# Kernel tuning notes

Hardware: AMD Instinct MI355X
Metric: run time of the kernel (lower is better)

The kernel has to match this reference:

```python
import jax, jax.numpy as jnp
import numpy as np
import math

D_MODEL = 1024
NHEAD = 16
D_FF = 4096
MAX_LEN = 512
LN_EPS = 1e-5


def setup_inputs() -> dict:
    key = jax.random.key(0)
    ks = jax.random.split(key, 12)
    d, h, dff, L = D_MODEL, NHEAD, D_FF, MAX_LEN
    B, S = 16, 512
    s = lambda k, shape, std: jax.random.normal(k, shape, dtype=jnp.float32) * std
    return {
        "x": s(ks[0], (B, S, d), 1.0),
        "in_proj_w": s(ks[1], (3 * d, d), d ** -0.5),   # torch MHA in_proj_weight
        "in_proj_b": jnp.zeros((3 * d,), jnp.float32),
        "out_w": s(ks[2], (d, d), d ** -0.5),            # out_proj.weight (out,in)
        "out_b": jnp.zeros((d,), jnp.float32),
        "rel_bias": s(ks[3], (h, 2 * L - 1), 0.02),      # (nhead, 2*max_len-1)
        "w1": s(ks[4], (dff, d), d ** -0.5),             # Linear(d, dff).weight
        "b1": jnp.zeros((dff,), jnp.float32),
        "w2": s(ks[5], (d, dff), dff ** -0.5),           # Linear(dff, d).weight
        "b2": jnp.zeros((d,), jnp.float32),
        "ln1_w": jnp.ones((d,), jnp.float32),
        "ln1_b": jnp.zeros((d,), jnp.float32),
        "ln2_w": jnp.ones((d,), jnp.float32),
        "ln2_b": jnp.zeros((d,), jnp.float32),
    }


def _layernorm(x, w, b):
    mu = jnp.mean(x, axis=-1, keepdims=True)
    var = jnp.mean(jnp.square(x - mu), axis=-1, keepdims=True)
    return (x - mu) * jax.lax.rsqrt(var + LN_EPS) * w + b


def _rel_pos_bias(rel_bias, seq_len):
    pos = jnp.arange(seq_len)
    rel = pos[:, None] - pos[None, :] + (MAX_LEN - 1)        # (S,S)
    rel = jnp.clip(rel, 0, 2 * MAX_LEN - 2)
    return rel_bias[:, rel]                                  # (H,S,S)


def reference(x, in_proj_w, in_proj_b, out_w, out_b, rel_bias,
              w1, b1, w2, b2, ln1_w, ln1_b, ln2_w, ln2_b):
    B, S, d = x.shape
    h = NHEAD
    hd = d // h
    bias = _rel_pos_bias(rel_bias, S)[None]                  # (1,H,S,S)

    # --- attention block (pre-norm) ---
    residual = x
    xn = _layernorm(x, ln1_w, ln1_b)
    qkv = xn @ in_proj_w.T + in_proj_b                       # (B,S,3d)
    q, k, v = jnp.split(qkv, 3, axis=-1)
    q = q.reshape(B, S, h, hd).transpose(0, 2, 1, 3)         # (B,H,S,hd)
    k = k.reshape(B, S, h, hd).transpose(0, 2, 1, 3)
    v = v.reshape(B, S, h, hd).transpose(0, 2, 1, 3)
    scores = jnp.einsum('bhqd,bhkd->bhqk', q, k) / math.sqrt(hd) + bias
    probs = jax.nn.softmax(scores, axis=-1)
    attn = jnp.einsum('bhqk,bhkd->bhqd', probs, v)           # (B,H,S,hd)
    attn = attn.transpose(0, 2, 1, 3).reshape(B, S, d)
    attn = attn @ out_w.T + out_b
    x = residual + attn

    # --- FFN block (pre-norm) ---
    residual = x
    xn = _layernorm(x, ln2_w, ln2_b)
    hdn = jax.nn.gelu(xn @ w1.T + b1, approximate=False)
    x = residual + hdn @ w2.T + b2
    return x
```

## Files before the change

kernel.cpp:

```cpp
#include <hip/hip_runtime.h>
#include <hip/hip_bf16.h>
#include <stdint.h>

typedef __hip_bfloat16 bf16;
typedef __attribute__((ext_vector_type(8))) __bf16 bf16x8;
typedef __attribute__((ext_vector_type(4))) float f32x4;

#define D_MODEL 1024
#define NHEAD   16
#define HDIM    64
#define DFF     4096
#define BATCH   16
#define SEQ     512
#define MROWS   (BATCH*SEQ)

__device__ __forceinline__ float b2f_bits(unsigned short u) {
    return __uint_as_float(((unsigned)u) << 16);
}
__device__ __forceinline__ bf16 f2b(float v) { return __float2bfloat16(v); }
__device__ __forceinline__ unsigned short f2b_bits(float v) {
    bf16 t = __float2bfloat16(v);
    return *(unsigned short*)&t;
}
__device__ __forceinline__ void gll16(void* lds, const void* gsrc) {
    __builtin_amdgcn_global_load_lds(
        (const __attribute__((address_space(1))) unsigned*)gsrc,
        (__attribute__((address_space(3))) unsigned*)lds,
        16, 0, 0);
}
__device__ __forceinline__ float gelu_f(float u) {
    float z  = 0.7978845608028654f * (u + 0.044715f * u * u * u);
    float az = fabsf(z);
    float e  = __expf(-2.0f * az);
    float th = (1.0f - e) / (1.0f + e);
    th = copysignf(th, z);
    return 0.5f * u * (1.0f + th);
}

__global__ __launch_bounds__(256)
void cvt_kernel(const float* __restrict__ in, bf16* __restrict__ out, int n)
{
    int i = (blockIdx.x * 256 + threadIdx.x) * 4;
    if (i >= n) return;
    float4 f = *(const float4*)(in + i);
    ushort4 o;
    o.x = f2b_bits(f.x); o.y = f2b_bits(f.y);
    o.z = f2b_bits(f.z); o.w = f2b_bits(f.w);
    *(ushort4*)((unsigned short*)out + i) = o;
}

__global__ __launch_bounds__(256)
void ln_kernel(const float* __restrict__ xin, const float* __restrict__ w,
               const float* __restrict__ b, bf16* __restrict__ out)
{
    int row  = blockIdx.x;
    int t    = threadIdx.x;
    int lane = t & 63, wv = t >> 6;
    int col  = t * 4;

    float4 f = *(const float4*)(xin + (size_t)row * D_MODEL + col);
    float v[4] = {f.x, f.y, f.z, f.w};

    float s  = v[0] + v[1] + v[2] + v[3];
    float ss = v[0]*v[0] + v[1]*v[1] + v[2]*v[2] + v[3]*v[3];
    #pragma unroll
    for (int m = 1; m < 64; m <<= 1) {
        s  += __shfl_xor(s,  m, 64);
        ss += __shfl_xor(ss, m, 64);
    }
    __shared__ float rs0[4], rs1[4];
    if (lane == 0) { rs0[wv] = s; rs1[wv] = ss; }
    __syncthreads();
    s  = rs0[0] + rs0[1] + rs0[2] + rs0[3];
    ss = rs1[0] + rs1[1] + rs1[2] + rs1[3];

    float mu  = s * (1.0f / D_MODEL);
    float var = ss * (1.0f / D_MODEL) - mu * mu;
    float rs  = rsqrtf(var + 1e-5f);

    float4 wf = *(const float4*)(w + col);
    float4 bf = *(const float4*)(b + col);
    ushort4 o;
    o.x = f2b_bits((v[0]-mu)*rs*wf.x + bf.x);
    o.y = f2b_bits((v[1]-mu)*rs*wf.y + bf.y);
    o.z = f2b_bits((v[2]-mu)*rs*wf.z + bf.z);
    o.w = f2b_bits((v[3]-mu)*rs*wf.w + bf.w);
    *(ushort4*)((unsigned short*)out + (size_t)row * D_MODEL + col) = o;
}

template<int EPI, bool OUT_B16>
__global__ __launch_bounds__(256)
void gemm_bt(const bf16* __restrict__ A, const bf16* __restrict__ Bw,
             const float* __restrict__ bias, const float* __restrict__ resid,
             void* __restrict__ Cout, bf16* __restrict__ qb,
             bf16* __restrict__ ktb, bf16* __restrict__ vb,
             int M, int N, int K)
{
    int t    = threadIdx.x;
    int lane = t & 63, w = t >> 6;
    int wm   = w & 1,  wn = w >> 1;
    int q    = lane >> 4, r = lane & 15;

    int gx  = gridDim.x;
    int L   = blockIdx.y * gx + blockIdx.x;
    int qq  = (gx * gridDim.y) >> 3;
    int nid = (L & 7) * qq + (L >> 3);
    int mb  = (nid / gx) * 128, nb = (nid % gx) * 128;

    __shared__ char smem[32768];

    f32x4 acc[4][4] = {};

    const char* Ag = (const char*)((const unsigned short*)A + (size_t)mb * K);
    const char* Bg = (const char*)((const unsigned short*)Bw + (size_t)nb * K);

    int ar0 = t >> 2,  ac0 = (t & 3) << 3;

    int nt = K >> 5;

    #define STAGE(c, k0) do {                                      \
        char* dA = smem + (c) * 16384;                             \
        char* dB = dA + 8192;                                      \
        size_t off0 = ((size_t)ar0 * K + (k0) + ac0) * 2;          \
        size_t off1 = off0 + (size_t)64 * K * 2;                   \
        gll16(dA + t * 16,        Ag + off0);                      \
        gll16(dA + 4096 + t * 16, Ag + off1);                      \
        gll16(dB + t * 16,        Bg + off0);                      \
        gll16(dB + 4096 + t * 16, Bg + off1);                      \
    } while (0)

    STAGE(0, 0);
    __syncthreads();

    int cur = 0;
    for (int tt = 0; tt < nt; ++tt) {
        if (tt + 1 < nt) STAGE(cur ^ 1, (tt + 1) << 5);

        const __bf16* Asb = (const __bf16*)(smem + cur * 16384);
        const __bf16* Bsb = Asb + 4096;
        bf16x8 af[4], bfr[4];
        #pragma unroll
        for (int i = 0; i < 4; i++)
            af[i] = *(const bf16x8*)(Asb + (wm * 64 + i * 16 + r) * 32 + q * 8);
        #pragma unroll
        for (int j = 0; j < 4; j++)
            bfr[j] = *(const bf16x8*)(Bsb + (wn * 64 + j * 16 + r) * 32 + q * 8);
        #pragma unroll
        for (int i = 0; i < 4; i++)
            #pragma unroll
            for (int j = 0; j < 4; j++)
                acc[i][j] = __builtin_amdgcn_mfma_f32_16x16x32_bf16(af[i], bfr[j], acc[i][j], 0, 0, 0);

        __syncthreads();
        cur ^= 1;
    }
    #undef STAGE

    if (OUT_B16 && EPI != 3) {
        __bf16* Cs = (__bf16*)smem;
        #pragma unroll
        for (int j = 0; j < 4; j++) {
            int n = nb + wn * 64 + j * 16 + r;
            float bv = bias[n];
            #pragma unroll
            for (int i = 0; i < 4; i++) {
                #pragma unroll
                for (int rr = 0; rr < 4; rr++) {
                    float v = acc[i][j][rr] + bv;
                    if (EPI == 1) v = gelu_f(v);
                    if (EPI == 2) v += resid[(size_t)(mb + wm*64 + i*16 + q*4 + rr) * N + n];
                    unsigned short ub = f2b_bits(v);
                    Cs[(wm*64 + i*16 + q*4 + rr) * 128 + wn*64 + j*16 + r] = *(__bf16*)&ub;
                }
            }
        }
        __syncthreads();
        char* Cg = (char*)Cout;
        #pragma unroll
        for (int c = 0; c < 8; c++) {
            int idx = t + c * 256;
            int row = idx >> 4, ch = idx & 15;
            *(int4*)(Cg + ((size_t)(mb + row) * N + nb) * 2 + ch * 16) =
                *(const int4*)((const char*)Cs + row * 256 + ch * 16);
        }
    } else {
        #pragma unroll
        for (int j = 0; j < 4; j++) {
            int n = nb + wn * 64 + j * 16 + r;
            float bv = bias[n];
            #pragma unroll
            for (int i = 0; i < 4; i++) {
                int mbase = mb + wm * 64 + i * 16 + q * 4;
                #pragma unroll
                for (int rr = 0; rr < 4; rr++) {
                    int m = mbase + rr;
                    float v = acc[i][j][rr] + bv;
                    if (EPI == 1) v = gelu_f(v);
                    if (EPI == 2) v += resid[(size_t)m * N + n];
                    if (EPI == 3) {
                        int sect = n >> 10;
                        int h = (n >> 6) & 15;
                        int e = n & 63;
                        int bi = m >> 9, s = m & 511;
                        size_t bh = (size_t)bi * NHEAD + h;
                        bf16 val = f2b(v);
                        if (sect == 0)      qb[((bh * SEQ + s) << 6) + e] = val;
                        else if (sect == 1) ktb[((bh * SEQ + s) << 6) + e] = val;
                        else                vb[((bh * HDIM + e) << 9) + s] = val;
                    } else {
                        if (OUT_B16) ((bf16*)Cout)[(size_t)m * N + n] = f2b(v);
                        else         ((float*)Cout)[(size_t)m * N + n] = v;
                    }
                }
            }
        }
    }
}

__global__ __launch_bounds__(256, 3)
void attn_mfma(const bf16* __restrict__ Q, const bf16* __restrict__ K,
               const bf16* __restrict__ VT, const float* __restrict__ relb,
               bf16* __restrict__ out)
{
    int L   = blockIdx.x + (blockIdx.y << 3);
    int xcd = L & 7, jj = L >> 3;
    int bh  = xcd * 32 + (jj >> 3);
    int q0  = (jj & 7) * 64;
    int b   = bh >> 4, h = bh & 15;
    int t = threadIdx.x, lane = t & 63, w = t >> 6;
    int l15 = lane & 15, l4 = lane >> 4;

    __shared__ int4  kvbuf4[2048];
    __shared__ int4  Pls4[512];
    __shared__ float rbs[1024];

    char* kv = (char*)kvbuf4;
    char* Pb = (char*)Pls4;
    const char* Kg = (const char*)K  + ((size_t)bh << 16);
    const char* Vg = (const char*)VT + ((size_t)bh << 16);

    #define STAGE_KV(bs, c) do {                                              \
        char* kd = kv + (bs) * 16384;                                         \
        char* vd = kd + 8192;                                                 \
        _Pragma("unroll")                                                     \
        for (int i = 0; i < 2; i++) {                                         \
            int g = t + i * 256;                                              \
            int rr_ = g >> 3;                                                 \
            int jj_ = (g & 7) ^ (rr_ & 7);                                    \
            gll16(kd + g * 16,                                                \
                  Kg + (((size_t)(c) * 64 + rr_) << 7) + (jj_ << 4));         \
            gll16(vd + g * 16,                                                \
                  Vg + ((size_t)rr_ << 10) + ((size_t)(c) << 7) + (jj_ << 4));\
        }                                                                     \
    } while (0)

    const float* rb = relb + (size_t)h * (2 * SEQ - 1);
    for (int i = t; i < 2 * SEQ - 1; i += 256) rbs[i] = rb[i];
    STAGE_KV(0, 0);

    const unsigned short* Qp = (const unsigned short*)Q
        + (((size_t)bh * SEQ + q0 + w * 16 + l15) << 6) + l4 * 8;
    bf16x8 qf0 = *(const bf16x8*)Qp;
    bf16x8 qf1 = *(const bf16x8*)(Qp + 32);

    __syncthreads();

    int qbase  = q0 + w * 16 + l4 * 4;
    int prow   = w * 16 + l15;
    int prbase = prow << 7;
    int pswz   = (prow & 7) << 4;
    float sum[4] = {0.f, 0.f, 0.f, 0.f};
    f32x4 oacc[4] = {};

    int cur = 0;
    for (int c = 0; c < 8; ++c) {
        if (c < 7) STAGE_KV(cur ^ 1, c + 1);

        const char* Kl = kv + cur * 16384;
        const char* Vl = Kl + 8192;

        f32x4 sc[4];
        #pragma unroll
        for (int kt = 0; kt < 4; kt++) {
            int row = kt * 16 + l15;
            int swz = (row & 7) << 4;
            bf16x8 kf0 = *(const bf16x8*)(Kl + (((row << 7) + (l4 << 4)) ^ swz));
            bf16x8 kf1 = *(const bf16x8*)(Kl + (((row << 7) + 64 + (l4 << 4)) ^ swz));
            f32x4 a = {};
            a = __builtin_amdgcn_mfma_f32_16x16x32_bf16(qf0, kf0, a, 0, 0, 0);
            a = __builtin_amdgcn_mfma_f32_16x16x32_bf16(qf1, kf1, a, 0, 0, 0);
            sc[kt] = a;
        }

        #pragma unroll
        for (int kt = 0; kt < 4; kt++) {
            int relbase = qbase - (c * 64 + kt * 16 + l15) + (SEQ - 1);
            #pragma unroll
            for (int reg = 0; reg < 4; reg++) {
                float p = __expf(sc[kt][reg] * 0.125f + rbs[relbase + reg]);
                sum[reg] += p;
                float o = __shfl_xor(p, 1, 64);
                unsigned lo = f2b_bits((lane & 1) ? o : p);
                unsigned hi = f2b_bits((lane & 1) ? p : o);
                unsigned pk = lo | (hi << 16);
                if ((lane & 1) == (reg >> 1)) {
                    int row  = w * 16 + l4 * 4 + reg;
                    int byte = ((row << 7) + (kt << 5) + ((l15 & ~1) << 1))
                             ^ ((row & 7) << 4);
                    *(unsigned*)(Pb + byte) = pk;
                }
            }
        }

        #pragma unroll
        for (int k2 = 0; k2 < 2; k2++) {
            int pbyte = (prbase + (k2 << 6) + (l4 << 4)) ^ pswz;
            bf16x8 pf = *(const bf16x8*)(Pb + pbyte);
            #pragma unroll
            for (int et = 0; et < 4; et++) {
                int vrow = et * 16 + l15;
                bf16x8 vf = *(const bf16x8*)
                    (Vl + (((vrow << 7) + (k2 << 6) + (l4 << 4)) ^ ((vrow & 7) << 4)));
                oacc[et] = __builtin_amdgcn_mfma_f32_16x16x32_bf16(pf, vf, oacc[et], 0, 0, 0);
            }
        }

        __syncthreads();
        cur ^= 1;
    }
    #undef STAGE_KV

    #pragma unroll
    for (int m = 1; m < 16; m <<= 1)
        #pragma unroll
        for (int reg = 0; reg < 4; reg++)
            sum[reg] += __shfl_xor(sum[reg], m, 64);
    float rcp[4];
    #pragma unroll
    for (int reg = 0; reg < 4; reg++) rcp[reg] = 1.0f / sum[reg];

    bf16* op = out + (size_t)(b * SEQ + q0 + w * 16 + l4 * 4) * D_MODEL
             + h * HDIM + l15;
    #pragma unroll
    for (int et = 0; et < 4; et++)
        #pragma unroll
        for (int reg = 0; reg < 4; reg++)
            op[(size_t)reg * D_MODEL + et * 16] = f2b(oacc[et][reg] * rcp[reg]);
}

extern "C" void kernel_launch(void* const* d_in, const int* in_sizes, int n_in,
                              void* d_out, int out_size, void* d_ws, size_t ws_size,
                              hipStream_t stream)
{
    const float* x    = (const float*)d_in[0];
    const float* wqkv = (const float*)d_in[1];
    const float* bqkv = (const float*)d_in[2];
    const float* wo   = (const float*)d_in[3];
    const float* bo   = (const float*)d_in[4];
    const float* relb = (const float*)d_in[5];
    const float* w1   = (const float*)d_in[6];
    const float* b1   = (const float*)d_in[7];
    const float* w2   = (const float*)d_in[8];
    const float* b2   = (const float*)d_in[9];
    const float* ln1w = (const float*)d_in[10];
    const float* ln1b = (const float*)d_in[11];
    const float* ln2w = (const float*)d_in[12];
    const float* ln2b = (const float*)d_in[13];

    char* ws = (char*)d_ws;
    const size_t MB = 1048576;
    bf16*  wqkv_b = (bf16*)(ws + 1 * MB);
    bf16*  wo_b   = (bf16*)(ws + 7 * MB);
    bf16*  xn     = (bf16*)(ws + 9 * MB);
    bf16*  Qb     = (bf16*)(ws + 25 * MB);
    bf16*  Kb     = (bf16*)(ws + 41 * MB);
    float* x1     = (float*)(ws + 25 * MB);
    bf16*  w1_b   = (bf16*)(ws + 1 * MB);
    bf16*  w2_b   = (bf16*)(ws + 9 * MB);
    bf16*  xn2    = (bf16*)(ws + 9 * MB);
    bf16*  hid    = (bf16*)(ws + 57 * MB);
    bf16*  VT     = (bf16*)d_out;
    bf16*  att    = (bf16*)((char*)d_out + 16 * MB);
    float* out    = (float*)d_out;

    cvt_kernel<<<3072, 256, 0, stream>>>(wqkv, wqkv_b, 3 * D_MODEL * D_MODEL);
    cvt_kernel<<<1024, 256, 0, stream>>>(wo,   wo_b,   D_MODEL * D_MODEL);
    ln_kernel<<<MROWS, 256, 0, stream>>>(x, ln1w, ln1b, xn);
    gemm_bt<3,true><<<dim3(24, 64), 256, 0, stream>>>(xn, wqkv_b, bqkv, nullptr,
        nullptr, Qb, Kb, VT, MROWS, 3 * D_MODEL, D_MODEL);
    attn_mfma<<<dim3(8, 256), 256, 0, stream>>>(Qb, Kb, VT, relb, att);
    gemm_bt<2,false><<<dim3(8, 64), 256, 0, stream>>>(att, wo_b, bo, x,
        x1, nullptr, nullptr, nullptr, MROWS, D_MODEL, D_MODEL);
    cvt_kernel<<<4096, 256, 0, stream>>>(w1, w1_b, DFF * D_MODEL);
    ln_kernel<<<MROWS, 256, 0, stream>>>(x1, ln2w, ln2b, xn2);
    gemm_bt<1,true><<<dim3(32, 64), 256, 0, stream>>>(xn2, w1_b, b1, nullptr,
        hid, nullptr, nullptr, nullptr, MROWS, DFF, D_MODEL);
    cvt_kernel<<<4096, 256, 0, stream>>>(w2, w2_b, D_MODEL * DFF);
    gemm_bt<2,false><<<dim3(8, 64), 256, 0, stream>>>(hid, w2_b, b2, x1,
        out, nullptr, nullptr, nullptr, MROWS, D_MODEL, DFF);
}
```

Baseline: 518.4 us.

## Add 256x256-tile 8-wave GEMM with swizzled LDS for QKV and FFN1

Introduces a new GEMM kernel with 256x256 block tiles, 512 threads, double-buffered 128KB LDS, an XOR-swizzled LDS layout and interleaved half-tile prefetch with s_setprio around MFMA bursts. It replaces the 128x128 kernel for the QKV projection and the FFN first layer. The aim is more data reuse per LDS load, fewer bank conflicts and better overlap of loads with MFMA. In exchange, the large LDS footprint and high register use limit occupancy, and fewer blocks cover the grid.

Result: slower. 664.4 us (+28.2%).

```diff
diff --git a/kernel.cpp b/kernel.cpp
--- a/kernel.cpp
+++ b/kernel.cpp
@@ -88,13 +88,199 @@
     *(ushort4*)((unsigned short*)out + (size_t)row * D_MODEL + col) = o;
 }
 
+template<int EPI>
+__global__ __launch_bounds__(512, 2)
+void gemm8(const bf16* __restrict__ A, const bf16* __restrict__ Bw,
+           const float* __restrict__ bias, void* __restrict__ Cout,
+           bf16* __restrict__ qb, bf16* __restrict__ ktb,
+           bf16* __restrict__ vb, int M, int N, int K)
+{
+    constexpr int BUFSZ = 65536;
+    __shared__ char smem[131072];
+
+    int t = threadIdx.x;
+    int lane = t & 63, wid = t >> 6;
+    int wm = wid >> 2, wn = wid & 3;
+    int r = lane & 15, q = lane >> 4;
+
+    int gx  = gridDim.x;
+    int L   = blockIdx.y * gx + blockIdx.x;
+    int qq  = (gx * gridDim.y) >> 3;
+    int nid = (L & 7) * qq + (L >> 3);
+    int mb  = (nid / gx) * 256, nb = (nid % gx) * 256;
+
+    const char* Ag = (const char*)A + (size_t)mb * K * 2;
+    const char* Bg = (const char*)Bw + (size_t)nb * K * 2;
+
+    int g0r = t >> 2,   g0j = (t & 3) ^ ((g0r >> 1) & 3);
+    int g1r = g0r + 128, g1j = (t & 3) ^ ((g1r >> 1) & 3);
+    size_t a0 = (size_t)g0r * K * 2 + (size_t)g0j * 16;
+    size_t a1 = (size_t)g1r * K * 2 + (size_t)g1j * 16;
+
+    #define STG(mat, h, T, b) do {                                       \
+        char* d = smem + (b) * BUFSZ + (mat) * 32768 + (h) * 16384;      \
+        const char* s = (mat) ? Bg : Ag;                                 \
+        size_t ko = ((size_t)(T) * 64 + (h) * 32) * 2;                   \
+        gll16(d + t * 16,        s + a0 + ko);                           \
+        gll16(d + 8192 + t * 16, s + a1 + ko);                           \
+    } while (0)
+
+    f32x4 acc[8][4] = {};
+    int NT = K >> 6;
+    int rowA = wm * 128 + r;
+    int rowB = wn * 64 + r;
+
+    STG(0, 0, 0, 0); STG(1, 0, 0, 0); STG(0, 1, 0, 0); STG(1, 1, 0, 0);
+    asm volatile("s_waitcnt vmcnt(4)" ::: "memory");
+    __builtin_amdgcn_s_barrier();
+
+    for (int T = 0; T < NT; ++T) {
+        const char* Ab = smem + (T & 1) * BUFSZ;
+        const char* Bb = Ab + 32768;
+        bool pf = (T + 1 < NT);
+        int bn = (T & 1) ^ 1;
+
+        bf16x8 af[4], bfq[4];
+
+        if (pf) STG(0, 0, T + 1, bn);
+        #pragma unroll
+        for (int i = 0; i < 4; i++) {
+            int ro = rowA + i * 16;
+            af[i] = *(const bf16x8*)(Ab + ro * 64 + ((q ^ ((ro >> 1) & 3)) << 4));
+        }
+        #pragma unroll
+        for (int j = 0; j < 4; j++) {
+            int ro = rowB + j * 16;
+            bfq[j] = *(const bf16x8*)(Bb + ro * 64 + ((q ^ ((ro >> 1) & 3)) << 4));
+        }
+        __builtin_amdgcn_s_barrier();
+        __builtin_amdgcn_s_setprio(1);
+        #pragma unroll
+        for (int i = 0; i < 4; i++)
+            #pragma unroll
+            for (int j = 0; j < 4; j++)
+                acc[i][j] = __builtin_amdgcn_mfma_f32_16x16x32_bf16(af[i], bfq[j], acc[i][j], 0, 0, 0);
+        __builtin_amdgcn_s_setprio(0);
+        __builtin_amdgcn_s_barrier();
+
+        if (pf) STG(1, 0, T + 1, bn);
+        #pragma unroll
+        for (int i = 0; i < 4; i++) {
+            int ro = rowA + 64 + i * 16;
+            af[i] = *(const bf16x8*)(Ab + ro * 64 + ((q ^ ((ro >> 1) & 3)) << 4));
+        }
+        __builtin_amdgcn_s_barrier();
+        __builtin_amdgcn_s_setprio(1);
+        #pragma unroll
+        for (int i = 0; i < 4; i++)
+            #pragma unroll
+            for (int j = 0; j < 4; j++)
+                acc[i + 4][j] = __builtin_amdgcn_mfma_f32_16x16x32_bf16(af[i], bfq[j], acc[i + 4][j], 0, 0, 0);
+        __builtin_amdgcn_s_setprio(0);
+        asm volatile("s_waitcnt vmcnt(4)" ::: "memory");
+        __builtin_amdgcn_s_barrier();
+
+        if (pf) STG(0, 1, T + 1, bn);
+        #pragma unroll
+        for (int i = 0; i < 4; i++) {
+            int ro = rowA + i * 16;
+            af[i] = *(const bf16x8*)(Ab + 16384 + ro * 64 + ((q ^ ((ro >> 1) & 3)) << 4));
+        }
+        #pragma unroll
+        for (int j = 0; j < 4; j++) {
+            int ro = rowB + j * 16;
+            bfq[j] = *(const bf16x8*)(Bb + 16384 + ro * 64 + ((q ^ ((ro >> 1) & 3)) << 4));
+        }
+        __builtin_amdgcn_s_barrier();
+        __builtin_amdgcn_s_setprio(1);
+        #pragma unroll
+        for (int i = 0; i < 4; i++)
+            #pragma unroll
+            for (int j = 0; j < 4; j++)
+                acc[i][j] = __builtin_amdgcn_mfma_f32_16x16x32_bf16(af[i], bfq[j], acc[i][j], 0, 0, 0);
+        __builtin_amdgcn_s_setprio(0);
+        __builtin_amdgcn_s_barrier();
+
+        if (pf) STG(1, 1, T + 1, bn);
+        #pragma unroll
+        for (int i = 0; i < 4; i++) {
+            int ro = rowA + 64 + i * 16;
+            af[i] = *(const bf16x8*)(Ab + 16384 + ro * 64 + ((q ^ ((ro >> 1) & 3)) << 4));
+        }
+        __builtin_amdgcn_s_barrier();
+        __builtin_amdgcn_s_setprio(1);
+        #pragma unroll
+        for (int i = 0; i < 4; i++)
+            #pragma unroll
+            for (int j = 0; j < 4; j++)
+                acc[i + 4][j] = __builtin_amdgcn_mfma_f32_16x16x32_bf16(af[i], bfq[j], acc[i + 4][j], 0, 0, 0);
+        __builtin_amdgcn_s_setprio(0);
+        asm volatile("s_waitcnt vmcnt(4)" ::: "memory");
+        __builtin_amdgcn_s_barrier();
+    }
+    #undef STG
+
+    if (EPI == 1) {
+        asm volatile("s_waitcnt vmcnt(0)" ::: "memory");
+        __syncthreads();
+        __bf16* Cs = (__bf16*)smem;
+        char* Cg = (char*)Cout;
+        #pragma unroll
+        for (int hh = 0; hh < 2; ++hh) {
+            if (wm == hh) {
+                #pragma unroll
+                for (int j = 0; j < 4; j++) {
+                    int n = nb + wn * 64 + j * 16 + r;
+                    float bv = bias[n];
+                    #pragma unroll
+                    for (int i = 0; i < 8; i++)
+                        #pragma unroll
+                        for (int rr = 0; rr < 4; rr++) {
+                            float v = gelu_f(acc[i][j][rr] + bv);
+                            unsigned short ub = f2b_bits(v);
+                            Cs[(i * 16 + q * 4 + rr) * 256 + wn * 64 + j * 16 + r] = *(__bf16*)&ub;
+                        }
+                }
+            }
+            __syncthreads();
+            #pragma unroll
+            for (int p = 0; p < 8; p++) {
+                int idx = t + p * 512;
+                int lrow = idx >> 5, ch = idx & 31;
+                *(int4*)(Cg + ((size_t)(mb + hh * 128 + lrow) * N + nb) * 2 + ch * 16) =
+                    *(const int4*)((const char*)Cs + lrow * 512 + ch * 16);
+            }
+            __syncthreads();
+        }
+    } else {
+        #pragma unroll
+        for (int j = 0; j < 4; j++) {
+            int n = nb + wn * 64 + j * 16 + r;
+            float bv = bias[n];
+            int sect = n >> 10, h = (n >> 6) & 15, e = n & 63;
+            #pragma unroll
+            for (int i = 0; i < 8; i++) {
+                int mbase = mb + wm * 128 + i * 16 + q * 4;
+                #pragma unroll
+                for (int rr = 0; rr < 4; rr++) {
+                    int m = mbase + rr;
+                    int bi = m >> 9, s = m & 511;
+                    size_t bh = (size_t)bi * NHEAD + h;
+                    bf16 val = f2b(acc[i][j][rr] + bv);
+                    if (sect == 0)      qb[((bh * SEQ + s) << 6) + e] = val;
+                    else if (sect == 1) ktb[((bh * SEQ + s) << 6) + e] = val;
+                    else                vb[((bh * HDIM + e) << 9) + s] = val;
+                }
+            }
+        }
+    }
+}
+
 template<int EPI, bool OUT_B16>
 __global__ __launch_bounds__(256)
 void gemm_bt(const bf16* __restrict__ A, const bf16* __restrict__ Bw,
              const float* __restrict__ bias, const float* __restrict__ resid,
-             void* __restrict__ Cout, bf16* __restrict__ qb,
-             bf16* __restrict__ ktb, bf16* __restrict__ vb,
-             int M, int N, int K)
+             void* __restrict__ Cout, int M, int N, int K)
 {
     int t    = threadIdx.x;
     int lane = t & 63, w = t >> 6;
@@ -156,62 +342,21 @@
     }
     #undef STAGE
 
-    if (OUT_B16 && EPI != 3) {
-        __bf16* Cs = (__bf16*)smem;
-        #pragma unroll
-        for (int j = 0; j < 4; j++) {
-            int n = nb + wn * 64 + j * 16 + r;
-            float bv = bias[n];
-            #pragma unroll
-            for (int i = 0; i < 4; i++) {
-                #pragma unroll
-                for (int rr = 0; rr < 4; rr++) {
-                    float v = acc[i][j][rr] + bv;
-                    if (EPI == 1) v = gelu_f(v);
-                    if (EPI == 2) v += resid[(size_t)(mb + wm*64 + i*16 + q*4 + rr) * N + n];
-                    unsigned short ub = f2b_bits(v);
-                    Cs[(wm*64 + i*16 + q*4 + rr) * 128 + wn*64 + j*16 + r] = *(__bf16*)&ub;
-                }
-            }
-        }
-        __syncthreads();
-        char* Cg = (char*)Cout;
-        #pragma unroll
-        for (int c = 0; c < 8; c++) {
-            int idx = t + c * 256;
-            int row = idx >> 4, ch = idx & 15;
-            *(int4*)(Cg + ((size_t)(mb + row) * N + nb) * 2 + ch * 16) =
-                *(const int4*)((const char*)Cs + row * 256 + ch * 16);
-        }
-    } else {
-        #pragma unroll
-        for (int j = 0; j < 4; j++) {
-            int n = nb + wn * 64 + j * 16 + r;
-            float bv = bias[n];
-            #pragma unroll
-            for (int i = 0; i < 4; i++) {
-                int mbase = mb + wm * 64 + i * 16 + q * 4;
-                #pragma unroll
-                for (int rr = 0; rr < 4; rr++) {
-                    int m = mbase + rr;
-                    float v = acc[i][j][rr] + bv;
-                    if (EPI == 1) v = gelu_f(v);
-                    if (EPI == 2) v += resid[(size_t)m * N + n];
-                    if (EPI == 3) {
-                        int sect = n >> 10;
-                        int h = (n >> 6) & 15;
-                        int e = n & 63;
-                        int bi = m >> 9, s = m & 511;
-                        size_t bh = (size_t)bi * NHEAD + h;
-                        bf16 val = f2b(v);
-                        if (sect == 0)      qb[((bh * SEQ + s) << 6) + e] = val;
-                        else if (sect == 1) ktb[((bh * SEQ + s) << 6) + e] = val;
-                        else                vb[((bh * HDIM + e) << 9) + s] = val;
-                    } else {
-                        if (OUT_B16) ((bf16*)Cout)[(size_t)m * N + n] = f2b(v);
-                        else         ((float*)Cout)[(size_t)m * N + n] = v;
-                    }
-                }
+    #pragma unroll
+    for (int j = 0; j < 4; j++) {
+        int n = nb + wn * 64 + j * 16 + r;
+        float bv = bias[n];
+        #pragma unroll
+        for (int i = 0; i < 4; i++) {
+            int mbase = mb + wm * 64 + i * 16 + q * 4;
+            #pragma unroll
+            for (int rr = 0; rr < 4; rr++) {
+                int m = mbase + rr;
+                float v = acc[i][j][rr] + bv;
+                if (EPI == 1) v = gelu_f(v);
+                if (EPI == 2) v += resid[(size_t)m * N + n];
+                if (OUT_B16) ((bf16*)Cout)[(size_t)m * N + n] = f2b(v);
+                else         ((float*)Cout)[(size_t)m * N + n] = v;
             }
         }
     }
@@ -386,16 +531,16 @@
     cvt_kernel<<<3072, 256, 0, stream>>>(wqkv, wqkv_b, 3 * D_MODEL * D_MODEL);
     cvt_kernel<<<1024, 256, 0, stream>>>(wo,   wo_b,   D_MODEL * D_MODEL);
     ln_kernel<<<MROWS, 256, 0, stream>>>(x, ln1w, ln1b, xn);
-    gemm_bt<3,true><<<dim3(24, 64), 256, 0, stream>>>(xn, wqkv_b, bqkv, nullptr,
-        nullptr, Qb, Kb, VT, MROWS, 3 * D_MODEL, D_MODEL);
+    gemm8<3><<<dim3(12, 32), 512, 0, stream>>>(xn, wqkv_b, bqkv, nullptr,
+        Qb, Kb, VT, MROWS, 3 * D_MODEL, D_MODEL);
     attn_mfma<<<dim3(8, 256), 256, 0, stream>>>(Qb, Kb, VT, relb, att);
     gemm_bt<2,false><<<dim3(8, 64), 256, 0, stream>>>(att, wo_b, bo, x,
-        x1, nullptr, nullptr, nullptr, MROWS, D_MODEL, D_MODEL);
+        x1, MROWS, D_MODEL, D_MODEL);
     cvt_kernel<<<4096, 256, 0, stream>>>(w1, w1_b, DFF * D_MODEL);
     ln_kernel<<<MROWS, 256, 0, stream>>>(x1, ln2w, ln2b, xn2);
-    gemm_bt<1,true><<<dim3(32, 64), 256, 0, stream>>>(xn2, w1_b, b1, nullptr,
-        hid, nullptr, nullptr, nullptr, MROWS, DFF, D_MODEL);
+    gemm8<1><<<dim3(16, 32), 512, 0, stream>>>(xn2, w1_b, b1, hid,
+        nullptr, nullptr, nullptr, MROWS, DFF, D_MODEL);
     cvt_kernel<<<4096, 256, 0, stream>>>(w2, w2_b, D_MODEL * DFF);
     gemm_bt<2,false><<<dim3(8, 64), 256, 0, stream>>>(hid, w2_b, b2, x1,
-        out, nullptr, nullptr, nullptr, MROWS, D_MODEL, DFF);
-}
+        out, MROWS, D_MODEL, DFF);
+}
```

## Coalesce Q/K epilogue stores via LDS and read rel-bias from global in attention

Applied to the files above, without the earlier changes.

The QKV GEMM epilogue now stages the Q and K sections through shared memory and writes them with 16-byte vector stores, instead of scattered 2-byte stores. The V section keeps its transposed scalar stores. In the attention kernel, the 4 KB shared-memory copy of the relative-position bias is dropped and the bias is read directly from global memory (cached). This frees LDS, and the kernel's launch-bounds occupancy hint is raised from 3 to 4 blocks, at the cost of more global or cache loads inside the softmax loop.

Result: faster. 503.4 us (-2.9%).

```diff
diff --git a/kernel.cpp b/kernel.cpp
--- a/kernel.cpp
+++ b/kernel.cpp
@@ -156,7 +156,53 @@
     }
     #undef STAGE
 
-    if (OUT_B16 && EPI != 3) {
+    if (EPI == 3) {
+        if (nb < 2048) {
+            __bf16* Cs = (__bf16*)smem;
+            #pragma unroll
+            for (int j = 0; j < 4; j++) {
+                int n = nb + wn * 64 + j * 16 + r;
+                float bv = bias[n];
+                #pragma unroll
+                for (int i = 0; i < 4; i++)
+                    #pragma unroll
+                    for (int rr = 0; rr < 4; rr++) {
+                        unsigned short ub = f2b_bits(acc[i][j][rr] + bv);
+                        Cs[(wm*64 + i*16 + q*4 + rr) * 128 + wn*64 + j*16 + r] = *(__bf16*)&ub;
+                    }
+            }
+            __syncthreads();
+            bf16* dst = (nb >> 10) ? ktb : qb;
+            #pragma unroll
+            for (int p = 0; p < 8; p++) {
+                int idx = t + p * 256;
+                int row = idx >> 4, ch = idx & 15;
+                int n  = nb + ch * 8;
+                int hh = (n >> 6) & 15, e0 = n & 63;
+                int m  = mb + row, bi = m >> 9, s = m & 511;
+                *(int4*)(dst + ((((size_t)bi * 16 + hh) * 512 + s) << 6) + e0) =
+                    *(const int4*)(Cs + row * 128 + ch * 8);
+            }
+        } else {
+            #pragma unroll
+            for (int j = 0; j < 4; j++) {
+                int n = nb + wn * 64 + j * 16 + r;
+                float bv = bias[n];
+                int h = (n >> 6) & 15, e = n & 63;
+                #pragma unroll
+                for (int i = 0; i < 4; i++) {
+                    int mbase = mb + wm * 64 + i * 16 + q * 4;
+                    #pragma unroll
+                    for (int rr = 0; rr < 4; rr++) {
+                        int m = mbase + rr;
+                        int bi = m >> 9, s = m & 511;
+                        size_t bh = (size_t)bi * NHEAD + h;
+                        vb[((bh * HDIM + e) << 9) + s] = f2b(acc[i][j][rr] + bv);
+                    }
+                }
+            }
+        }
+    } else if (OUT_B16) {
         __bf16* Cs = (__bf16*)smem;
         #pragma unroll
         for (int j = 0; j < 4; j++) {
@@ -197,27 +243,14 @@
                     float v = acc[i][j][rr] + bv;
                     if (EPI == 1) v = gelu_f(v);
                     if (EPI == 2) v += resid[(size_t)m * N + n];
-                    if (EPI == 3) {
-                        int sect = n >> 10;
-                        int h = (n >> 6) & 15;
-                        int e = n & 63;
-                        int bi = m >> 9, s = m & 511;
-                        size_t bh = (size_t)bi * NHEAD + h;
-                        bf16 val = f2b(v);
-                        if (sect == 0)      qb[((bh * SEQ + s) << 6) + e] = val;
-                        else if (sect == 1) ktb[((bh * SEQ + s) << 6) + e] = val;
-                        else                vb[((bh * HDIM + e) << 9) + s] = val;
-                    } else {
-                        if (OUT_B16) ((bf16*)Cout)[(size_t)m * N + n] = f2b(v);
-                        else         ((float*)Cout)[(size_t)m * N + n] = v;
-                    }
+                    ((float*)Cout)[(size_t)m * N + n] = v;
                 }
             }
         }
     }
 }
 
-__global__ __launch_bounds__(256, 3)
+__global__ __launch_bounds__(256, 4)
 void attn_mfma(const bf16* __restrict__ Q, const bf16* __restrict__ K,
                const bf16* __restrict__ VT, const float* __restrict__ relb,
                bf16* __restrict__ out)
@@ -232,12 +265,12 @@
 
     __shared__ int4  kvbuf4[2048];
     __shared__ int4  Pls4[512];
-    __shared__ float rbs[1024];
 
     char* kv = (char*)kvbuf4;
     char* Pb = (char*)Pls4;
     const char* Kg = (const char*)K  + ((size_t)bh << 16);
     const char* Vg = (const char*)VT + ((size_t)bh << 16);
+    const float* rb = relb + (size_t)h * (2 * SEQ - 1);
 
     #define STAGE_KV(bs, c) do {                                              \
         char* kd = kv + (bs) * 16384;                                         \
@@ -254,8 +287,6 @@
         }                                                                     \
     } while (0)
 
-    const float* rb = relb + (size_t)h * (2 * SEQ - 1);
-    for (int i = t; i < 2 * SEQ - 1; i += 256) rbs[i] = rb[i];
     STAGE_KV(0, 0);
 
     const unsigned short* Qp = (const unsigned short*)Q
@@ -297,7 +328,7 @@
             int relbase = qbase - (c * 64 + kt * 16 + l15) + (SEQ - 1);
             #pragma unroll
             for (int reg = 0; reg < 4; reg++) {
-                float p = __expf(sc[kt][reg] * 0.125f + rbs[relbase + reg]);
+                float p = __expf(sc[kt][reg] * 0.125f + rb[relbase + reg]);
                 sum[reg] += p;
                 float o = __shfl_xor(p, 1, 64);
                 unsigned lo = f2b_bits((lane & 1) ? o : p);
```
